# Kernel optimization log

Hardware: AMD Instinct MI355X
Metric: run time of the kernel (lower is better)

The kernel has to match this reference:

```python
import jax, jax.numpy as jnp
import numpy as np

D = 1024
P = 10  # log2(D)
N = 16384


def _fft_idx(p, j):
    perm = np.arange(2 ** p)
    _mask = 2 ** (j + 1) - 1
    __mask = 2 ** j - 1
    mask_ = ~_mask
    perm_ = perm & mask_
    _perm = perm & _mask
    __perm = perm & __mask
    idx_uv = (__perm << 1) + (_perm >> j) + perm_
    idx_x = perm ^ 2 ** j
    return idx_uv, idx_x

# Static (P, D) permutation tables, computed once at import time.
_IDX_UV = np.stack([_fft_idx(P, j)[0] for j in range(P)])  # permutes UV vectors
_IDX_X = np.stack([_fft_idx(P, j)[1] for j in range(P)])   # permutes the input per stage
IDX_UV = jnp.asarray(_IDX_UV)


def _interleave(a, b):
    # a, b: (P, D//2) -> (P, D) with a at even slots, b at odd slots
    return jnp.stack([a, b], axis=-1).reshape(a.shape[0], -1)


def _uv_fft(theta, phi):
    # Deterministic UV_FFT (sigma_BS = 0, new=False path)
    s1 = jnp.sin(theta / 2)
    c1 = jnp.cos(theta / 2)
    s2 = jnp.sin(theta / 2 + phi)
    c2 = jnp.cos(theta / 2 + phi)
    u_re = _interleave(-s1 * s2, s1 ** 2)
    v_re = _interleave(-c1 * s1, -c1 * s2)
    u_im = _interleave(s1 * c2, -c1 * s1)
    v_im = _interleave(c1 ** 2, c1 * c2)
    # per-layer permutation of the UV vectors
    u_re = jnp.take_along_axis(u_re, IDX_UV, axis=1)
    v_re = jnp.take_along_axis(v_re, IDX_UV, axis=1)
    u_im = jnp.take_along_axis(u_im, IDX_UV, axis=1)
    v_im = jnp.take_along_axis(v_im, IDX_UV, axis=1)
    return u_re, v_re, u_im, v_im


def setup_inputs() -> dict:
    key = jax.random.key(0)
    k1, k2, k3, k4 = jax.random.split(key, 4)
    X = jax.random.normal(k1, (N, 2 * D), dtype=jnp.float32)
    theta = jnp.arcsin(jax.random.uniform(k2, (P, D // 2), dtype=jnp.float32))
    phi = jax.random.uniform(k3, (P, D // 2), dtype=jnp.float32) * (2 * np.pi)
    psi = jax.random.uniform(k4, (D,), dtype=jnp.float32) * (2 * np.pi)
    return {"X": X, "theta": theta, "phi": phi, "psi": psi}


def reference(X, theta, phi, psi):
    u_re, v_re, u_im, v_im = _uv_fft(theta, phi)
    Xr = X[:, :D]
    Xi = X[:, D:]
    # P = log2(D) sequential butterfly stages (small static unrolled loop)
    for j in range(P):
        perm = _IDX_X[j]  # static numpy index -> compiled gather
        sr = Xr[:, perm]
        si = Xi[:, perm]
        Yr = u_re[j] * Xr - u_im[j] * Xi + (v_re[j] * sr - v_im[j] * si)
        Yi = u_re[j] * Xi + u_im[j] * Xr + (v_re[j] * si + v_im[j] * sr)
        Xr, Xi = Yr, Yi
    # final diagonal phase layer (use_psi=True)
    cp = jnp.cos(psi)
    sp = jnp.sin(psi)
    Yr = cp * Xr - sp * Xi
    Yi = cp * Xi + sp * Xr
    return jnp.concatenate([Yr, Yi], axis=1)
```

## Files before the change

kernel.cpp:

```cpp
#include <hip/hip_runtime.h>
#include <hip/hip_fp16.h>

#define P 10
#define D 1024
#define NROWS 16384

typedef float nfloat4 __attribute__((ext_vector_type(4)));

__global__ void coef_kernel(const float* __restrict__ theta,
                            const float* __restrict__ phi,
                            const float* __restrict__ psi,
                            uint2* __restrict__ ctab) {
    int idx = blockIdx.x * blockDim.x + threadIdx.x;
    if (idx >= P * D) return;
    int j = idx >> 10;
    int slot = idx & (D - 1);
    int e = slot >> 6;
    int lane = slot & 63;
    int k = ((e >> 2) << 8) + (lane << 2) + (e & 3);
    int b = (k >> j) & 1;
    unsigned lowmask = (1u << j) - 1u;
    unsigned m = ((unsigned)k & lowmask) | (((unsigned)k >> 1) & ~lowmask);
    float th = theta[j * (D / 2) + m];
    float ph = phi[j * (D / 2) + m];
    float h = th * 0.5f;
    float s1 = sinf(h), c1 = cosf(h);
    float s2 = sinf(h + ph), c2 = cosf(h + ph);
    float ur, ui, vr, vi;
    if (b) { ur =  s1 * s1; vr = -c1 * s2; ui = -c1 * s1; vi = c1 * c2; }
    else   { ur = -s1 * s2; vr = -c1 * s1; ui =  s1 * c2; vi = c1 * c1; }
    if (j == P - 1) {
        float ps = psi[k];
        float cp = cosf(ps), sp = sinf(ps);
        float ur2 = cp * ur - sp * ui, ui2 = sp * ur + cp * ui;
        float vr2 = cp * vr - sp * vi, vi2 = sp * vr + cp * vi;
        ur = ur2; ui = ui2; vr = vr2; vi = vi2;
    }
    __half2 uh = __floats2half2_rn(ur, ui);
    __half2 vh = __floats2half2_rn(vr, vi);
    uint2 w;
    w.x = *reinterpret_cast<unsigned int*>(&uh);
    w.y = *reinterpret_cast<unsigned int*>(&vh);
    ctab[idx] = w;
}

__device__ __forceinline__ void unpack_c(uint2 w, float& ur, float& ui,
                                         float& vr, float& vi) {
    __half2 a = *reinterpret_cast<__half2*>(&w.x);
    __half2 b = *reinterpret_cast<__half2*>(&w.y);
    ur = __low2float(a); ui = __high2float(a);
    vr = __low2float(b); vi = __high2float(b);
}

template <int PM>
__device__ __forceinline__ void stage_intra(float (&ra)[16], float (&ia)[16],
                                            float (&rb)[16], float (&ib)[16],
                                            const uint2* cj) {
#pragma unroll
    for (int e0 = 0; e0 < 16; ++e0) {
        if (e0 & PM) continue;
        const int e1 = e0 | PM;
        uint2 w0 = cj[e0 * 64];
        uint2 w1 = cj[e1 * 64];
        float u0r, u0i, v0r, v0i, u1r, u1i, v1r, v1i;
        unpack_c(w0, u0r, u0i, v0r, v0i);
        unpack_c(w1, u1r, u1i, v1r, v1i);
        float ar0 = ra[e0], ai0 = ia[e0], ar1 = ra[e1], ai1 = ia[e1];
        float br0 = rb[e0], bi0 = ib[e0], br1 = rb[e1], bi1 = ib[e1];
        ra[e0] = u0r * ar0 - u0i * ai0 + v0r * ar1 - v0i * ai1;
        ia[e0] = u0r * ai0 + u0i * ar0 + v0r * ai1 + v0i * ar1;
        ra[e1] = u1r * ar1 - u1i * ai1 + v1r * ar0 - v1i * ai0;
        ia[e1] = u1r * ai1 + u1i * ar1 + v1r * ai0 + v1i * ar0;
        rb[e0] = u0r * br0 - u0i * bi0 + v0r * br1 - v0i * bi1;
        ib[e0] = u0r * bi0 + u0i * br0 + v0r * bi1 + v0i * br1;
        rb[e1] = u1r * br1 - u1i * bi1 + v1r * br0 - v1i * bi0;
        ib[e1] = u1r * bi1 + u1i * br1 + v1r * bi0 + v1i * br0;
    }
}

template <int MASK>
__device__ __forceinline__ void stage_shfl(float (&ra)[16], float (&ia)[16],
                                           float (&rb)[16], float (&ib)[16],
                                           const uint2* cj) {
#pragma unroll
    for (int e = 0; e < 16; ++e) {
        uint2 w = cj[e * 64];
        float ur, ui, vr, vi;
        unpack_c(w, ur, ui, vr, vi);
        float sra = __shfl_xor(ra[e], MASK);
        float sia = __shfl_xor(ia[e], MASK);
        float srb = __shfl_xor(rb[e], MASK);
        float sib = __shfl_xor(ib[e], MASK);
        float nra = ur * ra[e] - ui * ia[e] + vr * sra - vi * sia;
        float nia = ur * ia[e] + ui * ra[e] + vr * sia + vi * sra;
        float nrb = ur * rb[e] - ui * ib[e] + vr * srb - vi * sib;
        float nib = ur * ib[e] + ui * rb[e] + vr * sib + vi * srb;
        ra[e] = nra; ia[e] = nia; rb[e] = nrb; ib[e] = nib;
    }
}

__global__ __launch_bounds__(256) void fft_kernel(const float* __restrict__ X,
                                                  const uint2* __restrict__ ctab,
                                                  float* __restrict__ out) {
    const int lane = threadIdx.x & 63;
    const int wave = threadIdx.x >> 6;
    const long rowbase = (long)blockIdx.x * 8 + (long)wave * 2;
    const float* x0 = X + rowbase * 2048 + lane * 4;
    const float* x1 = x0 + 2048;
    const uint2* cb = ctab + lane;

    float ra[16], ia[16], rb[16], ib[16];
#pragma unroll
    for (int eh = 0; eh < 4; ++eh) {
        float4 v0r = *(const float4*)(x0 + eh * 256);
        float4 v0i = *(const float4*)(x0 + 1024 + eh * 256);
        float4 v1r = *(const float4*)(x1 + eh * 256);
        float4 v1i = *(const float4*)(x1 + 1024 + eh * 256);
        ra[eh * 4 + 0] = v0r.x; ra[eh * 4 + 1] = v0r.y; ra[eh * 4 + 2] = v0r.z; ra[eh * 4 + 3] = v0r.w;
        ia[eh * 4 + 0] = v0i.x; ia[eh * 4 + 1] = v0i.y; ia[eh * 4 + 2] = v0i.z; ia[eh * 4 + 3] = v0i.w;
        rb[eh * 4 + 0] = v1r.x; rb[eh * 4 + 1] = v1r.y; rb[eh * 4 + 2] = v1r.z; rb[eh * 4 + 3] = v1r.w;
        ib[eh * 4 + 0] = v1i.x; ib[eh * 4 + 1] = v1i.y; ib[eh * 4 + 2] = v1i.z; ib[eh * 4 + 3] = v1i.w;
    }

    stage_intra<1>(ra, ia, rb, ib, cb + 0 * D);
    stage_intra<2>(ra, ia, rb, ib, cb + 1 * D);

    stage_shfl<1>(ra, ia, rb, ib, cb + 2 * D);
    stage_shfl<2>(ra, ia, rb, ib, cb + 3 * D);
    stage_shfl<4>(ra, ia, rb, ib, cb + 4 * D);
    stage_shfl<8>(ra, ia, rb, ib, cb + 5 * D);
    stage_shfl<16>(ra, ia, rb, ib, cb + 6 * D);
    stage_shfl<32>(ra, ia, rb, ib, cb + 7 * D);

    stage_intra<4>(ra, ia, rb, ib, cb + 8 * D);
    stage_intra<8>(ra, ia, rb, ib, cb + 9 * D);

    float* o0 = out + rowbase * 2048 + lane * 4;
    float* o1 = o0 + 2048;
#pragma unroll
    for (int eh = 0; eh < 4; ++eh) {
        nfloat4 v0r = { ra[eh * 4 + 0], ra[eh * 4 + 1], ra[eh * 4 + 2], ra[eh * 4 + 3] };
        nfloat4 v0i = { ia[eh * 4 + 0], ia[eh * 4 + 1], ia[eh * 4 + 2], ia[eh * 4 + 3] };
        nfloat4 v1r = { rb[eh * 4 + 0], rb[eh * 4 + 1], rb[eh * 4 + 2], rb[eh * 4 + 3] };
        nfloat4 v1i = { ib[eh * 4 + 0], ib[eh * 4 + 1], ib[eh * 4 + 2], ib[eh * 4 + 3] };
        __builtin_nontemporal_store(v0r, (nfloat4*)(o0 + eh * 256));
        __builtin_nontemporal_store(v0i, (nfloat4*)(o0 + 1024 + eh * 256));
        __builtin_nontemporal_store(v1r, (nfloat4*)(o1 + eh * 256));
        __builtin_nontemporal_store(v1i, (nfloat4*)(o1 + 1024 + eh * 256));
    }
}

extern "C" void kernel_launch(void* const* d_in, const int* in_sizes, int n_in,
                              void* d_out, int out_size, void* d_ws, size_t ws_size,
                              hipStream_t stream) {
    const float* X     = (const float*)d_in[0];
    const float* theta = (const float*)d_in[1];
    const float* phi   = (const float*)d_in[2];
    const float* psi   = (const float*)d_in[3];
    uint2* ctab = (uint2*)d_ws;

    coef_kernel<<<(P * D + 255) / 256, 256, 0, stream>>>(theta, phi, psi, ctab);
    fft_kernel<<<NROWS / 8, 256, 0, stream>>>(X, ctab, (float*)d_out);
}
```

Baseline: 74.96 us.

## Stage butterfly coefficients in LDS and enlarge blocks to 512 threads

Copies the first eight stages of packed coefficients (64KB) into shared memory per block and serves those stage loads from LDS instead of global/L1. Block size doubles to 16 rows so the staging copy is amortized over more rows. The last two stages still read coefficients from global. The large LDS footprint limits resident blocks per CU and adds a barrier before compute.

```diff
diff --git a/kernel.cpp b/kernel.cpp
--- a/kernel.cpp
+++ b/kernel.cpp
@@ -52,10 +52,10 @@
     vr = __low2float(b); vi = __high2float(b);
 }
 
-template <int PM>
+template <int PM, typename PTR>
 __device__ __forceinline__ void stage_intra(float (&ra)[16], float (&ia)[16],
                                             float (&rb)[16], float (&ib)[16],
-                                            const uint2* cj) {
+                                            PTR cj) {
 #pragma unroll
     for (int e0 = 0; e0 < 16; ++e0) {
         if (e0 & PM) continue;
@@ -78,10 +78,10 @@
     }
 }
 
-template <int MASK>
+template <int MASK, typename PTR>
 __device__ __forceinline__ void stage_shfl(float (&ra)[16], float (&ia)[16],
                                            float (&rb)[16], float (&ib)[16],
-                                           const uint2* cj) {
+                                           PTR cj) {
 #pragma unroll
     for (int e = 0; e < 16; ++e) {
         uint2 w = cj[e * 64];
@@ -99,15 +99,23 @@
     }
 }
 
-__global__ __launch_bounds__(256) void fft_kernel(const float* __restrict__ X,
+__global__ __launch_bounds__(512) void fft_kernel(const float* __restrict__ X,
                                                   const uint2* __restrict__ ctab,
                                                   float* __restrict__ out) {
-    const int lane = threadIdx.x & 63;
-    const int wave = threadIdx.x >> 6;
-    const long rowbase = (long)blockIdx.x * 8 + (long)wave * 2;
+    __shared__ uint4 lds4[4096];
+    const int tid  = threadIdx.x;
+    const int lane = tid & 63;
+    const int wave = tid >> 6;
+    const long rowbase = (long)blockIdx.x * 16 + (long)wave * 2;
     const float* x0 = X + rowbase * 2048 + lane * 4;
     const float* x1 = x0 + 2048;
-    const uint2* cb = ctab + lane;
+
+    {
+        const uint4* g4 = (const uint4*)ctab;
+#pragma unroll
+        for (int i = 0; i < 8; ++i)
+            lds4[i * 512 + tid] = g4[i * 512 + tid];
+    }
 
     float ra[16], ia[16], rb[16], ib[16];
 #pragma unroll
@@ -122,18 +130,21 @@
         ib[eh * 4 + 0] = v1i.x; ib[eh * 4 + 1] = v1i.y; ib[eh * 4 + 2] = v1i.z; ib[eh * 4 + 3] = v1i.w;
     }
 
-    stage_intra<1>(ra, ia, rb, ib, cb + 0 * D);
-    stage_intra<2>(ra, ia, rb, ib, cb + 1 * D);
+    __syncthreads();
 
-    stage_shfl<1>(ra, ia, rb, ib, cb + 2 * D);
-    stage_shfl<2>(ra, ia, rb, ib, cb + 3 * D);
-    stage_shfl<4>(ra, ia, rb, ib, cb + 4 * D);
-    stage_shfl<8>(ra, ia, rb, ib, cb + 5 * D);
-    stage_shfl<16>(ra, ia, rb, ib, cb + 6 * D);
-    stage_shfl<32>(ra, ia, rb, ib, cb + 7 * D);
+    const uint2* lc = (const uint2*)lds4;
+    stage_intra<1>(ra, ia, rb, ib, lc + 0 * D + lane);
+    stage_intra<2>(ra, ia, rb, ib, lc + 1 * D + lane);
 
-    stage_intra<4>(ra, ia, rb, ib, cb + 8 * D);
-    stage_intra<8>(ra, ia, rb, ib, cb + 9 * D);
+    stage_shfl<1>(ra, ia, rb, ib, lc + 2 * D + lane);
+    stage_shfl<2>(ra, ia, rb, ib, lc + 3 * D + lane);
+    stage_shfl<4>(ra, ia, rb, ib, lc + 4 * D + lane);
+    stage_shfl<8>(ra, ia, rb, ib, lc + 5 * D + lane);
+    stage_shfl<16>(ra, ia, rb, ib, lc + 6 * D + lane);
+    stage_shfl<32>(ra, ia, rb, ib, lc + 7 * D + lane);
+
+    stage_intra<4>(ra, ia, rb, ib, ctab + 8 * D + lane);
+    stage_intra<8>(ra, ia, rb, ib, ctab + 9 * D + lane);
 
     float* o0 = out + rowbase * 2048 + lane * 4;
     float* o1 = o0 + 2048;
@@ -160,5 +171,5 @@
     uint2* ctab = (uint2*)d_ws;
 
     coef_kernel<<<(P * D + 255) / 256, 256, 0, stream>>>(theta, phi, psi, ctab);
-    fft_kernel<<<NROWS / 8, 256, 0, stream>>>(X, ctab, (float*)d_out);
+    fft_kernel<<<NROWS / 16, 512, 0, stream>>>(X, ctab, (float*)d_out);
 }
```

New measurement: 84.38 us. +12.6%, slower.
